# Performance work log

Hardware: AMD Instinct MI355X
Metric: run time of the kernel (lower is better)

Reference implementation:

```python
import jax, jax.numpy as jnp
import numpy as np

N_USERS = 200000
N_MOVIES = 80000
N = N_USERS + N_MOVIES
H = 64
F_MOVIE = 20
E = 1250000
EL = 500000


def setup_inputs() -> dict:
    key = jax.random.key(0)
    ks = jax.random.split(key, 13)
    s = 0.05
    inp = {
        "movie_x": jax.random.normal(ks[0], (N_MOVIES, F_MOVIE), jnp.float32),
        "user_emb": jax.random.normal(ks[1], (N_USERS, H), jnp.float32) * s,
        "movie_emb": jax.random.normal(ks[2], (N_MOVIES, H), jnp.float32) * s,
        "lin_W": jax.random.normal(ks[3], (H, F_MOVIE), jnp.float32) * s,
        "lin_b": jax.random.normal(ks[4], (H,), jnp.float32) * s,
        "W1l": jax.random.normal(ks[5], (H, H), jnp.float32) * s,
        "b1": jax.random.normal(ks[6], (H,), jnp.float32) * s,
        "W1r": jax.random.normal(ks[7], (H, H), jnp.float32) * s,
        "W2l": jax.random.normal(ks[8], (H, H), jnp.float32) * s,
        "b2": jax.random.normal(ks[9], (H,), jnp.float32) * s,
        "W2r": jax.random.normal(ks[10], (H, H), jnp.float32) * s,
        "edge_index": jax.random.randint(ks[11], (2, E), 0, N, jnp.int64),
        "edge_label_index": jnp.stack([
            jax.random.randint(jax.random.fold_in(ks[12], 0), (EL,), 0, N_USERS, jnp.int64),
            jax.random.randint(jax.random.fold_in(ks[12], 1), (EL,), 0, N_MOVIES, jnp.int64),
        ]),
    }
    return inp


def _sage(x, src, dst, Wl, bl, Wr):
    # PyG SAGEConv, mean aggregation: lin_l(mean_{j->i} x_j) + lin_r(x_i)
    msg = x[src]  # [E, H] gather
    agg = jax.ops.segment_sum(msg, dst, num_segments=N)  # [N, H] scatter-add
    deg = jax.ops.segment_sum(jnp.ones((src.shape[0],), x.dtype), dst, num_segments=N)
    mean = agg / jnp.maximum(deg, 1.0)[:, None]
    return mean @ Wl.T + bl + x @ Wr.T


def reference(movie_x, user_emb, movie_emb, lin_W, lin_b,
              W1l, b1, W1r, W2l, b2, W2r, edge_index, edge_label_index):
    # encode: users = embedding lookup (node_id == arange), movies = linear(x) + embedding
    x_user = user_emb
    x_movie = movie_x @ lin_W.T + lin_b + movie_emb
    x = jnp.concatenate([x_user, x_movie], axis=0)  # [N, H]

    src, dst = edge_index[0], edge_index[1]
    x = jax.nn.relu(_sage(x, src, dst, W1l, b1, W1r))
    x = _sage(x, src, dst, W2l, b2, W2r)

    xu = x[:N_USERS]
    xm = x[N_USERS:]
    # dot-product edge scoring over supervision edges
    u = xu[edge_label_index[0]]  # [EL, H]
    m = xm[edge_label_index[1]]  # [EL, H]
    return jnp.sum(u * m, axis=-1)  # [EL]
```

## Files before the change

### kernel.cpp

```cpp
#include <hip/hip_runtime.h>
#include <hip/hip_bf16.h>

#define NU 200000
#define NM 80000
#define NT 280000
#define HD 64
#define FM 20

#define BSHIFT 10
#define NBUCK ((NT + 1023) >> 10)
#define SCHUNK 4096

#define PD 72
#define PD8 (PD / 8)

typedef __attribute__((ext_vector_type(8))) short short8;
typedef __attribute__((ext_vector_type(4))) float floatx4;

__device__ __forceinline__ float bfu2f(unsigned short u) {
    union { unsigned int u; float f; } c; c.u = ((unsigned int)u) << 16; return c.f;
}

__device__ __forceinline__ unsigned short f2bf_raw(float f) {
    union { float f; unsigned int u; } c; c.f = f;
    unsigned int u = c.u + 0x7FFFu + ((c.u >> 16) & 1u);
    return (unsigned short)(u >> 16);
}

__device__ __forceinline__ float ldf(const void* p, long i, int isbf) {
    return isbf ? bfu2f(((const unsigned short*)p)[i]) : ((const float*)p)[i];
}
__device__ __forceinline__ int ldidx(const int* p, long j, int is64) {
    return is64 ? p[2 * j] : p[j];
}

__global__ void probe_kernel(const void* user_emb, const int* ei, int* flags) {
    int t = threadIdx.x;
    int bad = 0;
    for (int i = t; i < 128; i += 64) {
        unsigned short h = ((const unsigned short*)user_emb)[i];
        unsigned int e = (h >> 7) & 0xFF;
        if (e >= 135) bad = 1;
    }
    unsigned long long mf = __ballot(bad != 0);
    int odd_nonzero = 0;
    if (t < 16 && ei[2 * t + 1] != 0) odd_nonzero = 1;
    unsigned long long mi = __ballot(odd_nonzero != 0);
    if (t == 0) {
        flags[0] = (mf == 0) ? 1 : 0;
        flags[1] = (mi == 0) ? 1 : 0;
    }
}

__global__ __launch_bounds__(256) void prep_user(
    const void* __restrict__ user_emb,
    unsigned short* __restrict__ xb,
    const int* __restrict__ flags)
{
    long t = (long)blockIdx.x * 256 + threadIdx.x;
    int isbf = flags[0];
    if (isbf) {
        ((short8*)xb)[t] = ((const short8*)user_emb)[t];
    } else {
        floatx4 a = ((const floatx4*)user_emb)[2 * t];
        floatx4 b = ((const floatx4*)user_emb)[2 * t + 1];
        short8 r;
        r[0] = (short)f2bf_raw(a[0]); r[1] = (short)f2bf_raw(a[1]);
        r[2] = (short)f2bf_raw(a[2]); r[3] = (short)f2bf_raw(a[3]);
        r[4] = (short)f2bf_raw(b[0]); r[5] = (short)f2bf_raw(b[1]);
        r[6] = (short)f2bf_raw(b[2]); r[7] = (short)f2bf_raw(b[3]);
        ((short8*)xb)[t] = r;
    }
}

__global__ __launch_bounds__(256) void prep_movie(
    const void* __restrict__ movie_x,
    const void* __restrict__ movie_emb,
    const void* __restrict__ lin_W,
    const void* __restrict__ lin_b,
    unsigned short* __restrict__ xb,
    const int* __restrict__ flags)
{
    int isbf = flags[0];
    int tid = threadIdx.x;
    int lane = tid & 63;
    int wave = blockIdx.x * 4 + (tid >> 6);
    int m0 = __builtin_amdgcn_readfirstlane(wave << 2);
    if (m0 >= NM) return;

    float wr[FM];
    if (isbf) {
        const unsigned int* p = (const unsigned int*)((const unsigned short*)lin_W + (long)lane * FM);
        #pragma unroll
        for (int i = 0; i < FM / 2; ++i) {
            unsigned int u = p[i];
            wr[2 * i]     = bfu2f((unsigned short)(u & 0xFFFFu));
            wr[2 * i + 1] = bfu2f((unsigned short)(u >> 16));
        }
    } else {
        const floatx4* p = (const floatx4*)((const float*)lin_W + (long)lane * FM);
        #pragma unroll
        for (int i = 0; i < FM / 4; ++i) {
            floatx4 v = p[i];
            wr[4 * i] = v[0]; wr[4 * i + 1] = v[1]; wr[4 * i + 2] = v[2]; wr[4 * i + 3] = v[3];
        }
    }
    float bias = ldf(lin_b, lane, isbf);

    #pragma unroll
    for (int mm = 0; mm < 4; ++mm) {
        int m = m0 + mm;
        float a0 = bias + ldf(movie_emb, (long)m * HD + lane, isbf);
        float a1 = 0.f, a2 = 0.f, a3 = 0.f;
        if (isbf) {
            const unsigned int* mr = (const unsigned int*)((const unsigned short*)movie_x + (long)m * FM);
            #pragma unroll
            for (int kk = 0; kk < FM / 2; ++kk) {
                unsigned int u = mr[kk];
                float x0 = bfu2f((unsigned short)(u & 0xFFFFu));
                float x1 = bfu2f((unsigned short)(u >> 16));
                if (kk & 1) { a2 += x0 * wr[2 * kk]; a3 += x1 * wr[2 * kk + 1]; }
                else        { a0 += x0 * wr[2 * kk]; a1 += x1 * wr[2 * kk + 1]; }
            }
        } else {
            const float* mr = (const float*)movie_x + (long)m * FM;
            #pragma unroll
            for (int k = 0; k < FM; k += 4) {
                a0 += mr[k]     * wr[k];
                a1 += mr[k + 1] * wr[k + 1];
                a2 += mr[k + 2] * wr[k + 2];
                a3 += mr[k + 3] * wr[k + 3];
            }
        }
        xb[(long)(NU + m) * HD + lane] = f2bf_raw((a0 + a1) + (a2 + a3));
    }
}

__global__ __launch_bounds__(512) void blk_hist(
    const int* __restrict__ ei, int E,
    int* __restrict__ blkhist,
    const int* __restrict__ flags)
{
    __shared__ int h[NBUCK];
    int tid = threadIdx.x;
    for (int i = tid; i < NBUCK; i += 512) h[i] = 0;
    __syncthreads();
    int is64 = flags[1];
    long e0 = (long)blockIdx.x * SCHUNK;
    long e1 = e0 + SCHUNK; if (e1 > E) e1 = E;
    for (long j = e0 + tid; j < e1; j += 512) {
        int d = ldidx(ei, (long)E + j, is64);
        atomicAdd(&h[d >> BSHIFT], 1);
    }
    __syncthreads();
    long obase = (long)blockIdx.x * NBUCK;
    for (int i = tid; i < NBUCK; i += 512) blkhist[obase + i] = h[i];
}

__global__ __launch_bounds__(256) void col_scan(
    int* __restrict__ blkhist, int NSB,
    int* __restrict__ bcnt)
{
    __shared__ int larr[2048];
    __shared__ int lsum[256];
    int b = blockIdx.x;
    int t = threadIdx.x;
    for (int i = t; i < NSB; i += 256) larr[i] = blkhist[(long)i * NBUCK + b];
    __syncthreads();
    int C = (NSB + 255) >> 8;
    int beg = t * C;
    int end = beg + C; if (end > NSB) end = NSB; if (beg > NSB) beg = NSB;
    int s = 0;
    for (int i = beg; i < end; ++i) s += larr[i];
    lsum[t] = s;
    __syncthreads();
    for (int off = 1; off < 256; off <<= 1) {
        int v = lsum[t];
        if (t >= off) v += lsum[t - off];
        __syncthreads();
        lsum[t] = v;
        __syncthreads();
    }
    int run = (t == 0) ? 0 : lsum[t - 1];
    for (int i = beg; i < end; ++i) {
        int v = larr[i];
        blkhist[(long)i * NBUCK + b] = run;
        run += v;
    }
    if (t == 0) bcnt[b] = lsum[255];
}

__global__ __launch_bounds__(256) void bucket_scan(
    const int* __restrict__ bcnt, int* __restrict__ bstart, int E)
{
    __shared__ int s[256];
    int t = threadIdx.x;
    int a0 = (2 * t     < NBUCK) ? bcnt[2 * t]     : 0;
    int a1 = (2 * t + 1 < NBUCK) ? bcnt[2 * t + 1] : 0;
    s[t] = a0 + a1;
    __syncthreads();
    for (int off = 1; off < 256; off <<= 1) {
        int v = s[t];
        if (t >= off) v += s[t - off];
        __syncthreads();
        s[t] = v;
        __syncthreads();
    }
    int run = (t == 0) ? 0 : s[t - 1];
    if (2 * t     < NBUCK) bstart[2 * t]     = run;
    if (2 * t + 1 < NBUCK) bstart[2 * t + 1] = run + a0;
    if (t == 0) bstart[NBUCK] = E;
}

__global__ __launch_bounds__(512) void scatter_kernel(
    const int* __restrict__ ei, int E,
    const int* __restrict__ bstart,
    const int* __restrict__ blkhist,
    int* __restrict__ packed,
    const int* __restrict__ flags)
{
    __shared__ int cur[NBUCK];
    int tid = threadIdx.x;
    long obase = (long)blockIdx.x * NBUCK;
    for (int i = tid; i < NBUCK; i += 512) cur[i] = bstart[i] + blkhist[obase + i];
    __syncthreads();
    int is64 = flags[1];
    long e0 = (long)blockIdx.x * SCHUNK;
    long e1 = e0 + SCHUNK; if (e1 > E) e1 = E;
    for (long j = e0 + tid; j < e1; j += 512) {
        int s = ldidx(ei, j, is64);
        int d = ldidx(ei, (long)E + j, is64);
        int b = d >> BSHIFT;
        int pos = atomicAdd(&cur[b], 1);
        packed[pos] = (s << BSHIFT) | (d & ((1 << BSHIFT) - 1));
    }
}

__global__ __launch_bounds__(256) void finefill_kernel(
    const int* __restrict__ bstart,
    const int* __restrict__ packed,
    int* __restrict__ rowptr,
    int* __restrict__ cnt,
    int* __restrict__ srclist)
{
    __shared__ int lcnt[1 << BSHIFT];
    __shared__ int lsum[256];
    int b = blockIdx.x;
    int tid = threadIdx.x;
    int nbase = b << BSHIFT;
    int beg = bstart[b];
    int end = bstart[b + 1];

    for (int i = tid; i < (1 << BSHIFT); i += 256) lcnt[i] = 0;
    __syncthreads();

    for (int j = beg + tid; j < end; j += 256)
        atomicAdd(&lcnt[packed[j] & ((1 << BSHIFT) - 1)], 1);
    __syncthreads();

    int i0 = tid * 4;
    int c0 = lcnt[i0], c1 = lcnt[i0 + 1], c2 = lcnt[i0 + 2], c3 = lcnt[i0 + 3];
    lsum[tid] = c0 + c1 + c2 + c3;
    __syncthreads();
    for (int off = 1; off < 256; off <<= 1) {
        int v = lsum[tid];
        if (tid >= off) v += lsum[tid - off];
        __syncthreads();
        lsum[tid] = v;
        __syncthreads();
    }
    int run = beg + ((tid == 0) ? 0 : lsum[tid - 1]);
    int r0 = run, r1 = r0 + c0, r2 = r1 + c1, r3 = r2 + c2;

    int n0 = nbase + i0;
    if (n0     < NT) { rowptr[n0]     = r0; cnt[n0]     = c0; }
    if (n0 + 1 < NT) { rowptr[n0 + 1] = r1; cnt[n0 + 1] = c1; }
    if (n0 + 2 < NT) { rowptr[n0 + 2] = r2; cnt[n0 + 2] = c2; }
    if (n0 + 3 < NT) { rowptr[n0 + 3] = r3; cnt[n0 + 3] = c3; }

    lcnt[i0] = r0; lcnt[i0 + 1] = r1; lcnt[i0 + 2] = r2; lcnt[i0 + 3] = r3;
    __syncthreads();

    for (int j = beg + tid; j < end; j += 256) {
        int p = packed[j];
        int dl = p & ((1 << BSHIFT) - 1);
        int pos = atomicAdd(&lcnt[dl], 1);
        srclist[pos] = p >> BSHIFT;
    }
}

template <bool RELU>
__global__ __launch_bounds__(512) void sage_layer(
    const unsigned short* __restrict__ xin,
    const int* __restrict__ rowptr,
    const int* __restrict__ cnt,
    const int* __restrict__ srclist,
    const void* __restrict__ Wl,
    const void* __restrict__ bias,
    const void* __restrict__ Wr,
    unsigned short* __restrict__ xout,
    const int* __restrict__ flags)
{
    __shared__ short8 lWl8[HD * PD8];
    __shared__ short8 lWr8[HD * PD8];
    __shared__ short8 lm8[HD * PD8];
    __shared__ float lb[HD];

    int tid = threadIdx.x;
    int isbf = flags[0];

    if (isbf) {
        const short8* wl8 = (const short8*)Wl;
        const short8* wr8 = (const short8*)Wr;
        int i = tid;
        int di = (i >> 3) * PD8 + (i & 7);
        lWl8[di] = wl8[i];
        lWr8[di] = wr8[i];
    } else {
        const floatx4* wlf = (const floatx4*)Wl;
        const floatx4* wrf = (const floatx4*)Wr;
        int i = tid;
        int di = (i >> 3) * PD8 + (i & 7);
        floatx4 a = wlf[2 * i], b = wlf[2 * i + 1];
        short8 r;
        r[0]=(short)f2bf_raw(a[0]); r[1]=(short)f2bf_raw(a[1]); r[2]=(short)f2bf_raw(a[2]); r[3]=(short)f2bf_raw(a[3]);
        r[4]=(short)f2bf_raw(b[0]); r[5]=(short)f2bf_raw(b[1]); r[6]=(short)f2bf_raw(b[2]); r[7]=(short)f2bf_raw(b[3]);
        lWl8[di] = r;
        a = wrf[2 * i]; b = wrf[2 * i + 1];
        r[0]=(short)f2bf_raw(a[0]); r[1]=(short)f2bf_raw(a[1]); r[2]=(short)f2bf_raw(a[2]); r[3]=(short)f2bf_raw(a[3]);
        r[4]=(short)f2bf_raw(b[0]); r[5]=(short)f2bf_raw(b[1]); r[6]=(short)f2bf_raw(b[2]); r[7]=(short)f2bf_raw(b[3]);
        lWr8[di] = r;
    }
    if (tid < HD) lb[tid] = ldf(bias, tid, isbf);

    int tile = blockIdx.x;
    long base = (long)tile * HD * HD;

    int w8 = tid >> 6;
    int lane = tid & 63;
    int mrow = lane & 15;
    int quad = lane >> 4;
    int roww = (w8 & 3) * 16 + mrow;
    int htp  = w8 >> 2;

    const short8* xrow = (const short8*)&xin[base + (long)roww * HD];
    short8 ax0 = xrow[quad];
    short8 ax1 = xrow[quad + 4];

    int g = lane >> 3;
    int sub = lane & 7;
    int nl = w8 * 8 + g;
    int n = tile * 64 + nl;
    int beg = rowptr[n];
    int deg = cnt[n];

    float acc[8];
    #pragma unroll
    for (int k = 0; k < 8; ++k) acc[k] = 0.f;

    for (int j0 = 0; j0 < deg; j0 += 8) {
        int e = j0 + sub;
        int sv = (e < deg) ? srclist[beg + e] : 0;
        int cq = deg - j0; if (cq > 8) cq = 8;
        short8 r[8];
        #pragma unroll
        for (int q = 0; q < 8; ++q) {
            int s = __shfl(sv, (g << 3) | q);
            r[q] = *(const short8*)&xin[(long)s * HD + sub * 8];
        }
        #pragma unroll
        for (int q = 0; q < 8; ++q) {
            if (q < cq) {
                #pragma unroll
                for (int k = 0; k < 8; ++k)
                    acc[k] += bfu2f((unsigned short)r[q][k]);
            }
        }
    }

    float rd = 1.0f / fmaxf((float)deg, 1.0f);
    short8 o;
    #pragma unroll
    for (int k = 0; k < 8; ++k) o[k] = (short)f2bf_raw(acc[k] * rd);
    lm8[nl * PD8 + sub] = o;

    __syncthreads();

    short8 am0 = lm8[roww * PD8 + quad];
    short8 am1 = lm8[roww * PD8 + 4 + quad];

    floatx4 acc4[2];
    #pragma unroll
    for (int t = 0; t < 2; ++t) {
        int h = (htp * 2 + t) * 16 + mrow;
        short8 bl0 = lWl8[h * PD8 + quad];
        short8 bl1 = lWl8[h * PD8 + 4 + quad];
        short8 br0 = lWr8[h * PD8 + quad];
        short8 br1 = lWr8[h * PD8 + 4 + quad];
        floatx4 a = {0.f, 0.f, 0.f, 0.f};
        a = __builtin_amdgcn_mfma_f32_16x16x32_bf16(am0, bl0, a, 0, 0, 0);
        a = __builtin_amdgcn_mfma_f32_16x16x32_bf16(am1, bl1, a, 0, 0, 0);
        a = __builtin_amdgcn_mfma_f32_16x16x32_bf16(ax0, br0, a, 0, 0, 0);
        a = __builtin_amdgcn_mfma_f32_16x16x32_bf16(ax1, br1, a, 0, 0, 0);
        acc4[t] = a;
    }

    #pragma unroll
    for (int t = 0; t < 2; ++t) {
        int h = (htp * 2 + t) * 16 + mrow;
        float bv = lb[h];
        #pragma unroll
        for (int r = 0; r < 4; ++r) {
            int node = (w8 & 3) * 16 + quad * 4 + r;
            float v = acc4[t][r] + bv;
            if (RELU) v = fmaxf(v, 0.0f);
            xout[base + node * HD + h] = f2bf_raw(v);
        }
    }
}

__global__ __launch_bounds__(256) void dot_kernel(
    const unsigned short* __restrict__ x2,
    const int* __restrict__ eli,
    void* __restrict__ out,
    int EL,
    const int* __restrict__ flags)
{
    int wid = (blockIdx.x * 256 + threadIdx.x) >> 6;
    long base = (long)wid * 16;
    if (base >= EL) return;
    int lane = threadIdx.x & 63;
    int isbf = flags[0];
    int is64 = flags[1];

    int idxv = 0;
    if (lane < 16)      idxv = ldidx(eli, base + lane, is64);
    else if (lane < 32) idxv = ldidx(eli, (long)EL + base + (lane - 16), is64);

    int e   = lane >> 2;
    int seg = lane & 3;
    int u = __shfl(idxv, e);
    int m = __shfl(idxv, 16 + e);

    const short8* up = (const short8*)(x2 + (long)u * HD + seg * 16);
    const short8* mp = (const short8*)(x2 + (long)(NU + m) * HD + seg * 16);
    short8 a0 = up[0], a1 = up[1];
    short8 b0 = mp[0], b1 = mp[1];

    float p = 0.f;
    #pragma unroll
    for (int j = 0; j < 8; ++j) {
        p += bfu2f((unsigned short)a0[j]) * bfu2f((unsigned short)b0[j]);
        p += bfu2f((unsigned short)a1[j]) * bfu2f((unsigned short)b1[j]);
    }
    p += __shfl_xor(p, 1);
    p += __shfl_xor(p, 2);

    if (seg == 0) {
        long g = base + e;
        if (isbf) ((unsigned short*)out)[g] = f2bf_raw(p);
        else      ((float*)out)[g] = p;
    }
}

extern "C" void kernel_launch(void* const* d_in, const int* in_sizes, int n_in,
                              void* d_out, int out_size, void* d_ws, size_t ws_size,
                              hipStream_t stream)
{
    const void* movie_x   = d_in[0];
    const void* user_emb  = d_in[1];
    const void* movie_emb = d_in[2];
    const void* lin_W     = d_in[3];
    const void* lin_b     = d_in[4];
    const void* W1l       = d_in[5];
    const void* b1        = d_in[6];
    const void* W1r       = d_in[7];
    const void* W2l       = d_in[8];
    const void* b2        = d_in[9];
    const void* W2r       = d_in[10];
    const int* ei  = (const int*)d_in[11];
    const int* eli = (const int*)d_in[12];
    int E  = in_sizes[11] / 2;
    int EL = in_sizes[12] / 2;

    const int NSB = (E + SCHUNK - 1) / SCHUNK;

    char* w = (char*)d_ws;
    unsigned short* xb0     = (unsigned short*)w;  w += (size_t)NT * HD * 2;
    unsigned short* xb1     = (unsigned short*)w;  w += (size_t)NT * HD * 2;
    int*            cnt     = (int*)w;             w += (size_t)NT * 4;
    int*            rowptr  = (int*)w;             w += (size_t)NT * 4;
    int*            srclist = (int*)w;             w += (size_t)E * 4;
    int*            packed  = (int*)w;             w += (size_t)E * 4;
    int*            bcnt    = (int*)w;             w += (size_t)(NBUCK + 1) * 4;
    int*            bstart  = (int*)w;             w += (size_t)(NBUCK + 1) * 4;
    int*            blkhist = (int*)w;             w += (size_t)NSB * NBUCK * 4;
    int*            flags   = (int*)w;

    const int user_blocks   = (NU * HD / 8) / 256;
    const int movie_blocks  = NM / 16;
    const int tile_blocks   = NT / 64;
    const int dot_blocks    = ((EL + 15) / 16 + 3) / 4;

    probe_kernel<<<1, 64, 0, stream>>>(user_emb, ei, flags);

    prep_user<<<user_blocks, 256, 0, stream>>>(user_emb, xb0, flags);
    prep_movie<<<movie_blocks, 256, 0, stream>>>(movie_x, movie_emb, lin_W, lin_b, xb0, flags);

    blk_hist<<<NSB, 512, 0, stream>>>(ei, E, blkhist, flags);
    col_scan<<<NBUCK, 256, 0, stream>>>(blkhist, NSB, bcnt);
    bucket_scan<<<1, 256, 0, stream>>>(bcnt, bstart, E);
    scatter_kernel<<<NSB, 512, 0, stream>>>(ei, E, bstart, blkhist, packed, flags);
    finefill_kernel<<<NBUCK, 256, 0, stream>>>(bstart, packed, rowptr, cnt, srclist);

    sage_layer<true><<<tile_blocks, 512, 0, stream>>>(xb0, rowptr, cnt, srclist, W1l, b1, W1r, xb1, flags);
    sage_layer<false><<<tile_blocks, 512, 0, stream>>>(xb1, rowptr, cnt, srclist, W2l, b2, W2r, xb0, flags);

    dot_kernel<<<dot_blocks, 256, 0, stream>>>(xb0, eli, d_out, EL, flags);
}
```

Baseline: 305.4 us.

## Prepack weights once, read user embeddings directly, and widen dot-kernel edges per wave

```diff
diff --git a/kernel.cpp b/kernel.cpp
--- a/kernel.cpp
+++ b/kernel.cpp
@@ -11,8 +11,7 @@
 #define NBUCK ((NT + 1023) >> 10)
 #define SCHUNK 4096
 
-#define PD 72
-#define PD8 (PD / 8)
+#define PD8 9
 
 typedef __attribute__((ext_vector_type(8))) short short8;
 typedef __attribute__((ext_vector_type(4))) float floatx4;
@@ -52,25 +51,51 @@
     }
 }
 
+__global__ __launch_bounds__(512) void prep_weights(
+    const void* __restrict__ W1l, const void* __restrict__ b1, const void* __restrict__ W1r,
+    const void* __restrict__ W2l, const void* __restrict__ b2, const void* __restrict__ W2r,
+    unsigned short* __restrict__ wsW,
+    float* __restrict__ wsb,
+    const int* __restrict__ flags)
+{
+    int t = threadIdx.x;
+    int isbf = flags[0];
+    const void* srcs[4] = {W1l, W1r, W2l, W2r};
+    #pragma unroll
+    for (int w = 0; w < 4; ++w) {
+        unsigned short* dst = wsW + w * (HD * HD);
+        if (isbf) {
+            ((short8*)dst)[t] = ((const short8*)srcs[w])[t];
+        } else {
+            floatx4 a = ((const floatx4*)srcs[w])[2 * t];
+            floatx4 b = ((const floatx4*)srcs[w])[2 * t + 1];
+            short8 r;
+            r[0]=(short)f2bf_raw(a[0]); r[1]=(short)f2bf_raw(a[1]); r[2]=(short)f2bf_raw(a[2]); r[3]=(short)f2bf_raw(a[3]);
+            r[4]=(short)f2bf_raw(b[0]); r[5]=(short)f2bf_raw(b[1]); r[6]=(short)f2bf_raw(b[2]); r[7]=(short)f2bf_raw(b[3]);
+            ((short8*)dst)[t] = r;
+        }
+    }
+    if (t < HD) {
+        wsb[t]      = ldf(b1, t, isbf);
+        wsb[HD + t] = ldf(b2, t, isbf);
+    }
+}
+
 __global__ __launch_bounds__(256) void prep_user(
     const void* __restrict__ user_emb,
     unsigned short* __restrict__ xb,
     const int* __restrict__ flags)
 {
+    if (flags[0]) return;
     long t = (long)blockIdx.x * 256 + threadIdx.x;
-    int isbf = flags[0];
-    if (isbf) {
-        ((short8*)xb)[t] = ((const short8*)user_emb)[t];
-    } else {
-        floatx4 a = ((const floatx4*)user_emb)[2 * t];
-        floatx4 b = ((const floatx4*)user_emb)[2 * t + 1];
-        short8 r;
-        r[0] = (short)f2bf_raw(a[0]); r[1] = (short)f2bf_raw(a[1]);
-        r[2] = (short)f2bf_raw(a[2]); r[3] = (short)f2bf_raw(a[3]);
-        r[4] = (short)f2bf_raw(b[0]); r[5] = (short)f2bf_raw(b[1]);
-        r[6] = (short)f2bf_raw(b[2]); r[7] = (short)f2bf_raw(b[3]);
-        ((short8*)xb)[t] = r;
-    }
+    floatx4 a = ((const floatx4*)user_emb)[2 * t];
+    floatx4 b = ((const floatx4*)user_emb)[2 * t + 1];
+    short8 r;
+    r[0] = (short)f2bf_raw(a[0]); r[1] = (short)f2bf_raw(a[1]);
+    r[2] = (short)f2bf_raw(a[2]); r[3] = (short)f2bf_raw(a[3]);
+    r[4] = (short)f2bf_raw(b[0]); r[5] = (short)f2bf_raw(b[1]);
+    r[6] = (short)f2bf_raw(b[2]); r[7] = (short)f2bf_raw(b[3]);
+    ((short8*)xb)[t] = r;
 }
 
 __global__ __launch_bounds__(256) void prep_movie(
@@ -290,48 +315,24 @@
 }
 
 template <bool RELU>
-__global__ __launch_bounds__(512) void sage_layer(
+__global__ __launch_bounds__(512, 8) void sage_layer(
     const unsigned short* __restrict__ xin,
+    const void* __restrict__ uemb,
+    int use_uemb,
     const int* __restrict__ rowptr,
     const int* __restrict__ cnt,
     const int* __restrict__ srclist,
-    const void* __restrict__ Wl,
-    const void* __restrict__ bias,
-    const void* __restrict__ Wr,
+    const unsigned short* __restrict__ wWl,
+    const float* __restrict__ wb,
+    const unsigned short* __restrict__ wWr,
     unsigned short* __restrict__ xout,
     const int* __restrict__ flags)
 {
-    __shared__ short8 lWl8[HD * PD8];
-    __shared__ short8 lWr8[HD * PD8];
     __shared__ short8 lm8[HD * PD8];
-    __shared__ float lb[HD];
 
     int tid = threadIdx.x;
     int isbf = flags[0];
-
-    if (isbf) {
-        const short8* wl8 = (const short8*)Wl;
-        const short8* wr8 = (const short8*)Wr;
-        int i = tid;
-        int di = (i >> 3) * PD8 + (i & 7);
-        lWl8[di] = wl8[i];
-        lWr8[di] = wr8[i];
-    } else {
-        const floatx4* wlf = (const floatx4*)Wl;
-        const floatx4* wrf = (const floatx4*)Wr;
-        int i = tid;
-        int di = (i >> 3) * PD8 + (i & 7);
-        floatx4 a = wlf[2 * i], b = wlf[2 * i + 1];
-        short8 r;
-        r[0]=(short)f2bf_raw(a[0]); r[1]=(short)f2bf_raw(a[1]); r[2]=(short)f2bf_raw(a[2]); r[3]=(short)f2bf_raw(a[3]);
-        r[4]=(short)f2bf_raw(b[0]); r[5]=(short)f2bf_raw(b[1]); r[6]=(short)f2bf_raw(b[2]); r[7]=(short)f2bf_raw(b[3]);
-        lWl8[di] = r;
-        a = wrf[2 * i]; b = wrf[2 * i + 1];
-        r[0]=(short)f2bf_raw(a[0]); r[1]=(short)f2bf_raw(a[1]); r[2]=(short)f2bf_raw(a[2]); r[3]=(short)f2bf_raw(a[3]);
-        r[4]=(short)f2bf_raw(b[0]); r[5]=(short)f2bf_raw(b[1]); r[6]=(short)f2bf_raw(b[2]); r[7]=(short)f2bf_raw(b[3]);
-        lWr8[di] = r;
-    }
-    if (tid < HD) lb[tid] = ldf(bias, tid, isbf);
+    const unsigned short* ub = (use_uemb && isbf) ? (const unsigned short*)uemb : xin;
 
     int tile = blockIdx.x;
     long base = (long)tile * HD * HD;
@@ -342,10 +343,6 @@
     int quad = lane >> 4;
     int roww = (w8 & 3) * 16 + mrow;
     int htp  = w8 >> 2;
-
-    const short8* xrow = (const short8*)&xin[base + (long)roww * HD];
-    short8 ax0 = xrow[quad];
-    short8 ax1 = xrow[quad + 4];
 
     int g = lane >> 3;
     int sub = lane & 7;
@@ -365,8 +362,11 @@
         short8 r[8];
         #pragma unroll
         for (int q = 0; q < 8; ++q) {
-            int s = __shfl(sv, (g << 3) | q);
-            r[q] = *(const short8*)&xin[(long)s * HD + sub * 8];
+            if (q < cq) {
+                int s = __shfl(sv, (g << 3) | q);
+                const unsigned short* bp = (s < NU) ? ub : xin;
+                r[q] = *(const short8*)&bp[(long)s * HD + sub * 8];
+            }
         }
         #pragma unroll
         for (int q = 0; q < 8; ++q) {
@@ -386,33 +386,34 @@
 
     __syncthreads();
 
+    int gn = tile * 64 + roww;
+    const unsigned short* bx = (gn < NU) ? ub : xin;
+    const short8* xr = (const short8*)&bx[(long)gn * HD];
+    short8 ax0 = xr[quad];
+    short8 ax1 = xr[quad + 4];
+
     short8 am0 = lm8[roww * PD8 + quad];
     short8 am1 = lm8[roww * PD8 + 4 + quad];
 
-    floatx4 acc4[2];
     #pragma unroll
     for (int t = 0; t < 2; ++t) {
         int h = (htp * 2 + t) * 16 + mrow;
-        short8 bl0 = lWl8[h * PD8 + quad];
-        short8 bl1 = lWl8[h * PD8 + 4 + quad];
-        short8 br0 = lWr8[h * PD8 + quad];
-        short8 br1 = lWr8[h * PD8 + 4 + quad];
+        const short8* pl = (const short8*)&wWl[h * HD];
+        const short8* pr = (const short8*)&wWr[h * HD];
+        short8 bl0 = pl[quad];
+        short8 bl1 = pl[quad + 4];
+        short8 br0 = pr[quad];
+        short8 br1 = pr[quad + 4];
         floatx4 a = {0.f, 0.f, 0.f, 0.f};
         a = __builtin_amdgcn_mfma_f32_16x16x32_bf16(am0, bl0, a, 0, 0, 0);
         a = __builtin_amdgcn_mfma_f32_16x16x32_bf16(am1, bl1, a, 0, 0, 0);
         a = __builtin_amdgcn_mfma_f32_16x16x32_bf16(ax0, br0, a, 0, 0, 0);
         a = __builtin_amdgcn_mfma_f32_16x16x32_bf16(ax1, br1, a, 0, 0, 0);
-        acc4[t] = a;
-    }
-
-    #pragma unroll
-    for (int t = 0; t < 2; ++t) {
-        int h = (htp * 2 + t) * 16 + mrow;
-        float bv = lb[h];
+        float bv = wb[h];
         #pragma unroll
         for (int r = 0; r < 4; ++r) {
             int node = (w8 & 3) * 16 + quad * 4 + r;
-            float v = acc4[t][r] + bv;
+            float v = a[r] + bv;
             if (RELU) v = fmaxf(v, 0.0f);
             xout[base + node * HD + h] = f2bf_raw(v);
         }
@@ -427,39 +428,42 @@
     const int* __restrict__ flags)
 {
     int wid = (blockIdx.x * 256 + threadIdx.x) >> 6;
-    long base = (long)wid * 16;
+    long base = (long)wid * 32;
     if (base >= EL) return;
     int lane = threadIdx.x & 63;
     int isbf = flags[0];
     int is64 = flags[1];
 
     int idxv = 0;
-    if (lane < 16)      idxv = ldidx(eli, base + lane, is64);
-    else if (lane < 32) idxv = ldidx(eli, (long)EL + base + (lane - 16), is64);
-
-    int e   = lane >> 2;
-    int seg = lane & 3;
-    int u = __shfl(idxv, e);
-    int m = __shfl(idxv, 16 + e);
-
-    const short8* up = (const short8*)(x2 + (long)u * HD + seg * 16);
-    const short8* mp = (const short8*)(x2 + (long)(NU + m) * HD + seg * 16);
-    short8 a0 = up[0], a1 = up[1];
-    short8 b0 = mp[0], b1 = mp[1];
+    long off = base + (lane & 31);
+    if (off < EL) idxv = (lane < 32) ? ldidx(eli, off, is64)
+                                     : ldidx(eli, (long)EL + off, is64);
+
+    int eidx = lane >> 1;
+    int half = lane & 1;
+    int u = __shfl(idxv, eidx);
+    int m = __shfl(idxv, 32 + eidx);
+    bool valid = (base + eidx) < EL;
+
+    const short8* up = (const short8*)(x2 + (long)u * HD + half * 32);
+    const short8* mp = (const short8*)(x2 + (long)(NU + m) * HD + half * 32);
+    short8 a0 = up[0], a1 = up[1], a2 = up[2], a3 = up[3];
+    short8 b0 = mp[0], b1 = mp[1], b2 = mp[2], b3 = mp[3];
 
     float p = 0.f;
     #pragma unroll
     for (int j = 0; j < 8; ++j) {
         p += bfu2f((unsigned short)a0[j]) * bfu2f((unsigned short)b0[j]);
         p += bfu2f((unsigned short)a1[j]) * bfu2f((unsigned short)b1[j]);
+        p += bfu2f((unsigned short)a2[j]) * bfu2f((unsigned short)b2[j]);
+        p += bfu2f((unsigned short)a3[j]) * bfu2f((unsigned short)b3[j]);
     }
     p += __shfl_xor(p, 1);
-    p += __shfl_xor(p, 2);
-
-    if (seg == 0) {
-        long g = base + e;
-        if (isbf) ((unsigned short*)out)[g] = f2bf_raw(p);
-        else      ((float*)out)[g] = p;
+
+    if (half == 0 && valid) {
+        long gidx = base + eidx;
+        if (isbf) ((unsigned short*)out)[gidx] = f2bf_raw(p);
+        else      ((float*)out)[gidx] = p;
     }
 }
 
@@ -495,14 +499,17 @@
     int*            bcnt    = (int*)w;             w += (size_t)(NBUCK + 1) * 4;
     int*            bstart  = (int*)w;             w += (size_t)(NBUCK + 1) * 4;
     int*            blkhist = (int*)w;             w += (size_t)NSB * NBUCK * 4;
+    unsigned short* wsW     = (unsigned short*)w;  w += (size_t)4 * HD * HD * 2;
+    float*          wsb     = (float*)w;           w += (size_t)2 * HD * 4;
     int*            flags   = (int*)w;
 
     const int user_blocks   = (NU * HD / 8) / 256;
     const int movie_blocks  = NM / 16;
     const int tile_blocks   = NT / 64;
-    const int dot_blocks    = ((EL + 15) / 16 + 3) / 4;
+    const int dot_blocks    = ((EL + 31) / 32 + 3) / 4;
 
     probe_kernel<<<1, 64, 0, stream>>>(user_emb, ei, flags);
+    prep_weights<<<1, 512, 0, stream>>>(W1l, b1, W1r, W2l, b2, W2r, wsW, wsb, flags);
 
     prep_user<<<user_blocks, 256, 0, stream>>>(user_emb, xb0, flags);
     prep_movie<<<movie_blocks, 256, 0, stream>>>(movie_x, movie_emb, lin_W, lin_b, xb0, flags);
@@ -513,8 +520,10 @@
     scatter_kernel<<<NSB, 512, 0, stream>>>(ei, E, bstart, blkhist, packed, flags);
     finefill_kernel<<<NBUCK, 256, 0, stream>>>(bstart, packed, rowptr, cnt, srclist);
 
-    sage_layer<true><<<tile_blocks, 512, 0, stream>>>(xb0, rowptr, cnt, srclist, W1l, b1, W1r, xb1, flags);
-    sage_layer<false><<<tile_blocks, 512, 0, stream>>>(xb1, rowptr, cnt, srclist, W2l, b2, W2r, xb0, flags);
+    sage_layer<true><<<tile_blocks, 512, 0, stream>>>(
+        xb0, user_emb, 1, rowptr, cnt, srclist, wsW, wsb, wsW + HD * HD, xb1, flags);
+    sage_layer<false><<<tile_blocks, 512, 0, stream>>>(
+        xb1, user_emb, 0, rowptr, cnt, srclist, wsW + 2 * HD * HD, wsb + HD, wsW + 3 * HD * HD, xb0, flags);
 
     dot_kernel<<<dot_blocks, 256, 0, stream>>>(xb0, eli, d_out, EL, flags);
 }
```

Measured after the change: 374.7 us. 1.23x slower.
